# Optimization experiments

Hardware: AMD Instinct MI355X
Metric: run time of the kernel (lower is better)

The kernel has to match this reference:

```python
import jax, jax.numpy as jnp
import numpy as np

B, T, H, NIN, NOUT = 16, 64, 256, 2, 2
ALPHA = 0.25       # alpha_time_scale
BETA = 0.1         # beta_time_scale
SIGMA_SYN = 0.002
PERT_SIGMA = 0.1   # neural-noise sigma used only at t == perturbed_time


def setup_inputs() -> dict:
    key = jax.random.key(0)
    ks = jax.random.split(key, 8)
    return {
        'input_signal': jax.random.normal(ks[0], (B, T, NIN), jnp.float32),
        'hidden': jax.random.normal(ks[1], (B, H), jnp.float32) * 0.1,
        'w_in': jax.random.normal(ks[2], (H, NIN), jnp.float32) / np.sqrt(NIN).astype(np.float32),
        'w_hh': jax.random.normal(ks[3], (H, H), jnp.float32) / np.sqrt(H).astype(np.float32),
        'b_hh': jnp.zeros((H,), jnp.float32),
        'w_out': jax.random.normal(ks[4], (NOUT, H), jnp.float32) / np.sqrt(H).astype(np.float32),
        'noise_pert': jax.random.normal(ks[5], (B, H), jnp.float32),
        'syn_noise': jax.random.normal(ks[6], (T, B, H, H), jnp.float32),
        'perturbed_time': 32,
    }


def reference(input_signal, hidden, w_in, w_hh, b_hh, w_out, noise_pert, syn_noise, perturbed_time):
    # input_signal: [B,T,NIN]; hidden: [B,H]; plasticity (beta != 0) + anti-Hebbian branch.
    dt = input_signal.dtype
    Bn, Tn, _ = input_signal.shape
    Hn = hidden.shape[1]
    alpha = jnp.full((Hn,), ALPHA, dt)            # broadcasts over last (hidden) axis
    beta = jnp.full((Hn,), BETA, dt)
    sqrt_alpha = jnp.sqrt(alpha)
    sqrt_beta = jnp.sqrt(beta)

    xs_in = jnp.moveaxis(input_signal, 1, 0)      # [T,B,NIN]
    # new_j starts at w_hh; different_j = new_j - w_hh == 0, so it is derived each step.
    new_j0 = jnp.broadcast_to(w_hh, (Bn, Hn, Hn)).astype(dt)

    def step(carry, xs):
        h, new_j = carry
        x_t, sn_t, t = xs
        act = jnp.tanh(h)                                      # [B,H]
        diff_j = new_j - w_hh                                  # [B,H,H]
        # torch.matmul(act.unsqueeze(1), different_j).squeeze(1)
        dj_act = jnp.einsum('bi,bij->bj', act, diff_j)
        tmp = x_t @ w_in.T + act @ w_hh.T + b_hh + dj_act      # [B,H]
        noise = jnp.where(t == perturbed_time,
                          noise_pert * PERT_SIGMA * sqrt_alpha,
                          jnp.zeros((), dt))
        h = (1.0 - alpha) * h + alpha * tmp + noise
        # anti-Hebbian: -outer(act, act) + randn * sigma_syn * sqrt(beta)
        add_w = -jnp.einsum('bi,bj->bij', act, act) + sn_t * SIGMA_SYN * sqrt_beta
        new_j = new_j + beta * add_w                           # beta broadcasts on last axis
        out = h @ w_out.T                                      # [B,NOUT]
        return (h, new_j), (h, out)

    (h_fin, new_j), (hid_list, out_list) = jax.lax.scan(
        step, (hidden, new_j0), (xs_in, syn_noise, jnp.arange(Tn)))
    # [T,B,*] -> [B,T,*], matching the final permute in torch
    return (jnp.moveaxis(hid_list, 0, 1), jnp.moveaxis(out_list, 0, 1), h_fin, new_j)
```

## Files before the change

kernel.cpp:

```cpp
#include <hip/hip_runtime.h>

#define BB 16
#define TT 64
#define HH 256
#define NSUB 16
#define NBLK (BB * NSUB)

#define OUT_OFF  (BB * TT * HH)
#define HFIN_OFF (OUT_OFF + BB * TT * 2)
#define NJ_OFF   (HFIN_OFF + BB * HH)

#define C_SN    6.324555320336759e-05f
#define C_NOISE 0.05f

typedef unsigned long long u64;
typedef unsigned int u32;

__device__ __forceinline__ void slot_put(u64* p, u64 v) {
    (void)__hip_atomic_exchange(p, v, __ATOMIC_RELAXED, __HIP_MEMORY_SCOPE_AGENT);
}
__device__ __forceinline__ u64 slot_get(u64* p) {
    return __hip_atomic_fetch_add(p, 0ull, __ATOMIC_RELAXED, __HIP_MEMORY_SCOPE_AGENT);
}
__device__ __forceinline__ u64 pack(u32 tag, float v) {
    return ((u64)tag << 32) | (u64)__float_as_uint(v);
}

__global__ __launch_bounds__(256) void rnn_all(
    const float* __restrict__ x,
    const float* __restrict__ h0,
    const float* __restrict__ w_in,
    const float* __restrict__ w_hh,
    const float* __restrict__ b_hh,
    const float* __restrict__ w_out,
    const float* __restrict__ nper,
    const float* __restrict__ sn,
    const int*   __restrict__ pt_ptr,
    float*       __restrict__ dout,
    u64*         __restrict__ ws)
{
    const int tid = threadIdx.x;
    const int bid = blockIdx.x;
    const int b   = bid >> 4;
    const int sub = bid & 15;
    const int j0  = sub * 16;
    const int q     = tid & 15;
    const int rbase = tid >> 4;
    const int jcol  = j0 + q;
    const int wv = tid >> 6, ln = tid & 63;

    __shared__ float s_h[2][HH];
    __shared__ float s_act[HH];
    __shared__ float s_red[4][16];
    __shared__ float s_o[4][2];
    __shared__ float s_x[2 * TT];
    __shared__ float s_wt[16][HH];

    u64* slotb = ws + (size_t)b * (2 * NSUB * 16);

    const int pt = *pt_ptr;

    for (int idx = tid; idx < 16 * HH; idx += 256)
        s_wt[idx >> 8][idx & 255] = w_hh[(size_t)(j0 + (idx >> 8)) * HH + (idx & 255)];
    s_h[0][tid] = h0[b * HH + tid];
    if (tid < 2 * TT) s_x[tid] = x[b * 2 * TT + tid];

    float win0 = 0.f, win1 = 0.f, bh = 0.f, npv = 0.f;
    if (tid < 16) {
        win0 = w_in[jcol * 2 + 0];
        win1 = w_in[jcol * 2 + 1];
        bh   = b_hh[jcol];
        npv  = nper[b * HH + jcol] * C_NOISE;
    }
    const float wo0 = w_out[tid], wo1 = w_out[HH + tid];
    __syncthreads();

    float M_loc[16];
    #pragma unroll
    for (int m = 0; m < 16; ++m) M_loc[m] = s_wt[q][rbase + 16 * m];

    float sreg[16];
    {
        const float* snp = sn + ((size_t)b * HH + rbase) * HH + jcol;
        #pragma unroll
        for (int m = 0; m < 16; ++m) sreg[m] = snp[(size_t)(16 * m) * HH];
    }

    for (int t = 0; t < TT; ++t) {
        const int cur = t & 1, nxt = cur ^ 1;
        const u32 tagw = (u32)(t + 1);

        s_act[tid] = tanhf(s_h[cur][tid]);
        __syncthreads();

        float p = 0.f;
        #pragma unroll
        for (int m = 0; m < 16; ++m) p += s_act[rbase + 16 * m] * M_loc[m];
        p += __shfl_xor(p, 16, 64);
        p += __shfl_xor(p, 32, 64);
        if (ln < 16) s_red[wv][ln] = p;
        __syncthreads();

        if (tid < 16) {
            const float dj  = s_red[0][q] + s_red[1][q] + s_red[2][q] + s_red[3][q];
            const float tmp = s_x[2 * t] * win0 + s_x[2 * t + 1] * win1 + bh + dj;
            const float hn  = 0.75f * s_h[cur][jcol] + 0.25f * tmp
                            + ((t == pt) ? npv : 0.f);
            s_h[nxt][jcol] = hn;
            dout[((size_t)b * TT + t) * HH + jcol] = hn;
            slot_put(slotb + (cur * NSUB + sub) * 16 + q, pack(tagw, hn));
        }

        const float acol = s_act[jcol];
        #pragma unroll
        for (int m = 0; m < 16; ++m)
            M_loc[m] += C_SN * sreg[m] - 0.1f * s_act[rbase + 16 * m] * acol;
        if (t + 1 < TT) {
            const float* snp = sn + (((size_t)(t + 1) * BB + b) * HH + rbase) * HH + jcol;
            #pragma unroll
            for (int m = 0; m < 16; ++m) sreg[m] = snp[(size_t)(16 * m) * HH];
        }
        if (sub == 1) {
            float p0 = s_h[cur][tid] * wo0, p1 = s_h[cur][tid] * wo1;
            #pragma unroll
            for (int off = 32; off; off >>= 1) {
                p0 += __shfl_down(p0, off, 64);
                p1 += __shfl_down(p1, off, 64);
            }
            if (ln == 0) { s_o[wv][0] = p0; s_o[wv][1] = p1; }
        }

        if (tid < 240) {
            int fs = tid >> 4; fs += (fs >= sub);
            u64* sp = slotb + (cur * NSUB + fs) * 16 + (tid & 15);
            u64 v;
            for (;;) {
                v = slot_get(sp);
                if ((u32)(v >> 32) == tagw) break;
                v = slot_get(sp);
                if ((u32)(v >> 32) == tagw) break;
            }
            s_h[nxt][fs * 16 + (tid & 15)] = __uint_as_float((u32)v);
        }
        __syncthreads();

        if (sub == 1 && tid == 0 && t > 0) {
            dout[OUT_OFF + ((size_t)b * TT + (t - 1)) * 2 + 0] =
                s_o[0][0] + s_o[1][0] + s_o[2][0] + s_o[3][0];
            dout[OUT_OFF + ((size_t)b * TT + (t - 1)) * 2 + 1] =
                s_o[0][1] + s_o[1][1] + s_o[2][1] + s_o[3][1];
        }
    }

    if (sub == 1) {
        float p0 = s_h[0][tid] * wo0, p1 = s_h[0][tid] * wo1;
        #pragma unroll
        for (int off = 32; off; off >>= 1) {
            p0 += __shfl_down(p0, off, 64);
            p1 += __shfl_down(p1, off, 64);
        }
        if (ln == 0) { s_o[wv][0] = p0; s_o[wv][1] = p1; }
        __syncthreads();
        if (tid == 0) {
            dout[OUT_OFF + ((size_t)b * TT + (TT - 1)) * 2 + 0] =
                s_o[0][0] + s_o[1][0] + s_o[2][0] + s_o[3][0];
            dout[OUT_OFF + ((size_t)b * TT + (TT - 1)) * 2 + 1] =
                s_o[0][1] + s_o[1][1] + s_o[2][1] + s_o[3][1];
        }
    }
    if (sub == 2) dout[HFIN_OFF + b * HH + tid] = s_h[0][tid];

    #pragma unroll
    for (int m = 0; m < 16; ++m) {
        const int i = rbase + 16 * m;
        dout[NJ_OFF + ((size_t)b * HH + i) * HH + jcol] =
            w_hh[(size_t)i * HH + jcol] + M_loc[m] - s_wt[q][i];
    }
}

extern "C" void kernel_launch(void* const* d_in, const int* in_sizes, int n_in,
                              void* d_out, int out_size, void* d_ws, size_t ws_size,
                              hipStream_t stream) {
    (void)in_sizes; (void)n_in; (void)out_size; (void)ws_size;
    const float* x     = (const float*)d_in[0];
    const float* h0    = (const float*)d_in[1];
    const float* w_in  = (const float*)d_in[2];
    const float* w_hh  = (const float*)d_in[3];
    const float* b_hh  = (const float*)d_in[4];
    const float* w_out = (const float*)d_in[5];
    const float* nper  = (const float*)d_in[6];
    const float* sn    = (const float*)d_in[7];
    const int*   pt    = (const int*)d_in[8];
    float* dout        = (float*)d_out;
    u64* ws            = (u64*)d_ws;

    hipMemsetAsync(d_ws, 0, (size_t)BB * 2 * NSUB * 16 * sizeof(u64), stream);

    rnn_all<<<dim3(NBLK), dim3(256), 0, stream>>>(
        x, h0, w_in, w_hh, b_hh, w_out, nper, sn, pt, dout, ws);
}
```

Measured before the change: 143.0 us.

## Compute tanh at slot receipt into transposed double-buffered act array, drop one barrier

The tanh of each hidden element is now computed when the value arrives (by the owner thread or by the slot-polling thread) and stored into a double-buffered, transposed activation array. This removes the per-step tanh pass and its __syncthreads, and lets each thread load its 16 activations as four float4 reads. Each block's own hidden slice is kept in a register, and the poll loop keeps four atomic loads in flight. The cost is a double-buffered activation array, extra tanh work on the polling threads, and a more complex spin loop that adds atomic traffic.

Result: no change. 142.8 us (-0.1%).

```diff
diff --git a/kernel.cpp b/kernel.cpp
--- a/kernel.cpp
+++ b/kernel.cpp
@@ -49,35 +49,39 @@
     const int jcol  = j0 + q;
     const int wv = tid >> 6, ln = tid & 63;
 
+    __shared__ float s_actT[2][HH];
     __shared__ float s_h[2][HH];
-    __shared__ float s_act[HH];
     __shared__ float s_red[4][16];
     __shared__ float s_o[4][2];
     __shared__ float s_x[2 * TT];
     __shared__ float s_wt[16][HH];
 
     u64* slotb = ws + (size_t)b * (2 * NSUB * 16);
-
     const int pt = *pt_ptr;
 
     for (int idx = tid; idx < 16 * HH; idx += 256)
         s_wt[idx >> 8][idx & 255] = w_hh[(size_t)(j0 + (idx >> 8)) * HH + (idx & 255)];
-    s_h[0][tid] = h0[b * HH + tid];
+    {
+        const float hv = h0[b * HH + tid];
+        s_h[0][tid] = hv;
+        s_actT[0][(tid & 15) * 16 + (tid >> 4)] = tanhf(hv);
+    }
     if (tid < 2 * TT) s_x[tid] = x[b * 2 * TT + tid];
 
-    float win0 = 0.f, win1 = 0.f, bh = 0.f, npv = 0.f;
+    float wi0 = 0.f, wi1 = 0.f, bh = 0.f, npv = 0.f, hreg = 0.f;
     if (tid < 16) {
-        win0 = w_in[jcol * 2 + 0];
-        win1 = w_in[jcol * 2 + 1];
+        wi0  = w_in[jcol * 2 + 0];
+        wi1  = w_in[jcol * 2 + 1];
         bh   = b_hh[jcol];
         npv  = nper[b * HH + jcol] * C_NOISE;
+        hreg = h0[b * HH + jcol];
     }
     const float wo0 = w_out[tid], wo1 = w_out[HH + tid];
     __syncthreads();
 
-    float M_loc[16];
+    float M[16];
     #pragma unroll
-    for (int m = 0; m < 16; ++m) M_loc[m] = s_wt[q][rbase + 16 * m];
+    for (int m = 0; m < 16; ++m) M[m] = s_wt[q][rbase + 16 * m];
 
     float sreg[16];
     {
@@ -90,38 +94,44 @@
         const int cur = t & 1, nxt = cur ^ 1;
         const u32 tagw = (u32)(t + 1);
 
-        s_act[tid] = tanhf(s_h[cur][tid]);
-        __syncthreads();
-
+        float a[16];
+        #pragma unroll
+        for (int mq = 0; mq < 4; ++mq) {
+            float4 v = *(const float4*)&s_actT[cur][rbase * 16 + mq * 4];
+            a[mq * 4 + 0] = v.x; a[mq * 4 + 1] = v.y;
+            a[mq * 4 + 2] = v.z; a[mq * 4 + 3] = v.w;
+        }
         float p = 0.f;
         #pragma unroll
-        for (int m = 0; m < 16; ++m) p += s_act[rbase + 16 * m] * M_loc[m];
+        for (int m = 0; m < 16; ++m) p += a[m] * M[m];
         p += __shfl_xor(p, 16, 64);
         p += __shfl_xor(p, 32, 64);
         if (ln < 16) s_red[wv][ln] = p;
         __syncthreads();
 
         if (tid < 16) {
-            const float dj  = s_red[0][q] + s_red[1][q] + s_red[2][q] + s_red[3][q];
-            const float tmp = s_x[2 * t] * win0 + s_x[2 * t + 1] * win1 + bh + dj;
-            const float hn  = 0.75f * s_h[cur][jcol] + 0.25f * tmp
-                            + ((t == pt) ? npv : 0.f);
-            s_h[nxt][jcol] = hn;
-            dout[((size_t)b * TT + t) * HH + jcol] = hn;
-            slot_put(slotb + (cur * NSUB + sub) * 16 + q, pack(tagw, hn));
-        }
-
-        const float acol = s_act[jcol];
+            const float dj = s_red[0][tid] + s_red[1][tid]
+                           + s_red[2][tid] + s_red[3][tid];
+            const float tmp = s_x[2 * t] * wi0 + s_x[2 * t + 1] * wi1 + bh + dj;
+            hreg = 0.75f * hreg + 0.25f * tmp + ((t == pt) ? npv : 0.f);
+            slot_put(slotb + (cur * NSUB + sub) * 16 + tid, pack(tagw, hreg));
+            s_h[nxt][jcol] = hreg;
+            s_actT[nxt][q * 16 + sub] = tanhf(hreg);
+            dout[((size_t)b * TT + t) * HH + jcol] = hreg;
+        }
+
+        const float aj = s_actT[cur][q * 16 + sub];
         #pragma unroll
         for (int m = 0; m < 16; ++m)
-            M_loc[m] += C_SN * sreg[m] - 0.1f * s_act[rbase + 16 * m] * acol;
+            M[m] += C_SN * sreg[m] - 0.1f * a[m] * aj;
         if (t + 1 < TT) {
             const float* snp = sn + (((size_t)(t + 1) * BB + b) * HH + rbase) * HH + jcol;
             #pragma unroll
             for (int m = 0; m < 16; ++m) sreg[m] = snp[(size_t)(16 * m) * HH];
         }
         if (sub == 1) {
-            float p0 = s_h[cur][tid] * wo0, p1 = s_h[cur][tid] * wo1;
+            const float hv = s_h[cur][tid];
+            float p0 = hv * wo0, p1 = hv * wo1;
             #pragma unroll
             for (int off = 32; off; off >>= 1) {
                 p0 += __shfl_down(p0, off, 64);
@@ -132,15 +142,20 @@
 
         if (tid < 240) {
             int fs = tid >> 4; fs += (fs >= sub);
-            u64* sp = slotb + (cur * NSUB + fs) * 16 + (tid & 15);
+            const int fq = tid & 15;
+            u64* sp = slotb + (cur * NSUB + fs) * 16 + fq;
             u64 v;
+            u64 a0 = slot_get(sp), a1 = slot_get(sp),
+                a2 = slot_get(sp), a3 = slot_get(sp);
             for (;;) {
-                v = slot_get(sp);
-                if ((u32)(v >> 32) == tagw) break;
-                v = slot_get(sp);
-                if ((u32)(v >> 32) == tagw) break;
+                if ((u32)(a0 >> 32) == tagw) { v = a0; break; } a0 = slot_get(sp);
+                if ((u32)(a1 >> 32) == tagw) { v = a1; break; } a1 = slot_get(sp);
+                if ((u32)(a2 >> 32) == tagw) { v = a2; break; } a2 = slot_get(sp);
+                if ((u32)(a3 >> 32) == tagw) { v = a3; break; } a3 = slot_get(sp);
             }
-            s_h[nxt][fs * 16 + (tid & 15)] = __uint_as_float((u32)v);
+            const float hr = __uint_as_float((u32)v);
+            s_h[nxt][fs * 16 + fq] = hr;
+            s_actT[nxt][fq * 16 + fs] = tanhf(hr);
         }
         __syncthreads();
 
@@ -153,7 +168,8 @@
     }
 
     if (sub == 1) {
-        float p0 = s_h[0][tid] * wo0, p1 = s_h[0][tid] * wo1;
+        const float hv = s_h[0][tid];
+        float p0 = hv * wo0, p1 = hv * wo1;
         #pragma unroll
         for (int off = 32; off; off >>= 1) {
             p0 += __shfl_down(p0, off, 64);
@@ -174,7 +190,7 @@
     for (int m = 0; m < 16; ++m) {
         const int i = rbase + 16 * m;
         dout[NJ_OFF + ((size_t)b * HH + i) * HH + jcol] =
-            w_hh[(size_t)i * HH + jcol] + M_loc[m] - s_wt[q][i];
+            w_hh[(size_t)i * HH + jcol] + M[m] - s_wt[q][i];
     }
 }
 
```
